# Kernel tuning notes

Measured on AMD Instinct MI355X. Metric: run time of the kernel, lower is better.

Reference implementation:

```python
import jax, jax.numpy as jnp
import numpy as np


def _reduce1(x):
    # x: [B, n, d] -> [B, 2d]; exists=max, forall=min over objects (exclude_self is a no-op for cnt=1)
    return jnp.concatenate([x.max(axis=1), x.min(axis=1)], axis=-1)


def _reduce2(x):
    # x: [B, n, n, d] -> [B, n, 2d]; exclude_self masks diagonal i==j (0 for exists/max, 1 for forall/min)
    n = x.shape[1]
    diag = jnp.eye(n, dtype=bool)[None, :, :, None]
    exists = jnp.where(diag, 0.0, x).max(axis=2)
    forall = jnp.where(diag, 1.0, x).min(axis=2)
    return jnp.concatenate([exists, forall], axis=-1)


def _layer(f0, f1, f2, p):
    # One LogicLayer step (breadth=2, minmax reducer, exclude_self, sigmoid norm, no hidden layers)
    W0, b0, W1, b1, W2, b2 = p
    B, n, d1 = f1.shape
    # order 0: [self, reduce(order1)]
    g0 = jnp.concatenate([f0, _reduce1(f1)], axis=-1)
    o0 = jax.nn.sigmoid(g0 @ W0 + b0)
    # order 1: [expand(order0), self, reduce(order2)]
    e0 = jnp.broadcast_to(f0[:, None, :], (B, n, f0.shape[-1]))
    g1 = jnp.concatenate([e0, f1, _reduce2(f2)], axis=-1)
    o1 = jax.nn.sigmoid(g1 @ W1 + b1)
    # order 2: [expand(order1), self] then Permutation(2) = cat(x, swap(i,j))
    e1 = jnp.broadcast_to(f1[:, :, None, :], (B, n, n, d1))
    g2 = jnp.concatenate([e1, f2], axis=-1)
    g2 = jnp.concatenate([g2, jnp.swapaxes(g2, 1, 2)], axis=-1)
    o2 = jax.nn.sigmoid(g2 @ W2 + b2)
    return o0, o1, o2


def setup_inputs() -> dict:
    key = jax.random.key(0)
    B, n = 4, 256
    d = [32, 64, 64]
    O = 128
    ks = iter(jax.random.split(key, 64))
    inp = {
        "x0": jax.random.uniform(next(ks), (B, d[0]), dtype=jnp.float32),
        "x1": jax.random.uniform(next(ks), (B, n, d[1]), dtype=jnp.float32),
        "x2": jax.random.uniform(next(ks), (B, n, n, d[2]), dtype=jnp.float32),
    }
    fan_ins = [
        (d[0] + 2 * d[1], d[0] + d[1] + 2 * d[2], 2 * (d[1] + d[2])),  # layer 0
        (O + 2 * O, O + O + 2 * O, 2 * (O + O)),                        # layer 1
        (O + 2 * O, O + O + 2 * O, 2 * (O + O)),                        # layer 2
    ]
    for l, fins in enumerate(fan_ins):
        for o, fin in enumerate(fins):
            inp[f"W{o}_{l}"] = jax.random.normal(next(ks), (fin, O), dtype=jnp.float32) / np.sqrt(fin).astype(np.float32)
            inp[f"b{o}_{l}"] = jnp.zeros((O,), dtype=jnp.float32)
    return inp


def reference(x0, x1, x2,
              W0_0, b0_0, W1_0, b1_0, W2_0, b2_0,
              W0_1, b0_1, W1_1, b1_1, W2_1, b2_1,
              W0_2, b0_2, W1_2, b1_2, W2_2, b2_2):
    f = (x0, x1, x2)
    for p in ((W0_0, b0_0, W1_0, b1_0, W2_0, b2_0),
              (W0_1, b0_1, W1_1, b1_1, W2_1, b2_1),
              (W0_2, b0_2, W1_2, b1_2, W2_2, b2_2)):
        f = _layer(*f, p)
    return f
```

## Files before the change

kernel.cpp:

```cpp
#include <hip/hip_runtime.h>
#include <hip/hip_bf16.h>
#include <cstdint>

#define NN 256
#define NB 4
#define OC 128

using bf16x8_t = __attribute__((ext_vector_type(8))) __bf16;
using f32x4_t  = __attribute__((ext_vector_type(4))) float;

typedef const __attribute__((address_space(1))) uint8_t* gptr1_t;
typedef __attribute__((address_space(3))) uint8_t* lptr3_t;

__device__ __forceinline__ void async_load16(const void* g, void* l) {
  __builtin_amdgcn_global_load_lds((gptr1_t)g, (lptr3_t)l, 16, 0, 0);
}

__device__ __forceinline__ float sigf(float x) {
  return 1.0f / (1.0f + __expf(-x));
}

__device__ __forceinline__ uint16_t f2bf_rne(float f) {
  uint32_t u = __float_as_uint(f);
  uint32_t r = (u + 0x7fffu + ((u >> 16) & 1u)) >> 16;
  return (uint16_t)r;
}

__global__ __launch_bounds__(256) void reduce2_l0_kernel(
    const float* __restrict__ x2, float* __restrict__ r2,
    uint16_t* __restrict__ x2bf) {
  const int bid = blockIdx.x;
  const int b = bid >> 8, i = bid & 255;
  const int tid = threadIdx.x;
  const int q = tid & 15, s = tid >> 4;
  const size_t rowbase = ((size_t)(b * NN + i) * NN) * 64 + q * 4;
  float mx0 = 0.f, mx1 = 0.f, mx2 = 0.f, mx3 = 0.f;
  float mn0 = 1.f, mn1 = 1.f, mn2 = 1.f, mn3 = 1.f;
  for (int j = s; j < NN; j += 16) {
    const float4 x = *(const float4*)(x2 + rowbase + (size_t)j * 64);
    uint2 pk;
    pk.x = (uint32_t)f2bf_rne(x.x) | ((uint32_t)f2bf_rne(x.y) << 16);
    pk.y = (uint32_t)f2bf_rne(x.z) | ((uint32_t)f2bf_rne(x.w) << 16);
    *(uint2*)(x2bf + rowbase + (size_t)j * 64) = pk;
    if (j != i) {
      mx0 = fmaxf(mx0, x.x); mx1 = fmaxf(mx1, x.y);
      mx2 = fmaxf(mx2, x.z); mx3 = fmaxf(mx3, x.w);
      mn0 = fminf(mn0, x.x); mn1 = fminf(mn1, x.y);
      mn2 = fminf(mn2, x.z); mn3 = fminf(mn3, x.w);
    }
  }
  __shared__ float4 smx[256], smn[256];
  smx[tid] = make_float4(mx0, mx1, mx2, mx3);
  smn[tid] = make_float4(mn0, mn1, mn2, mn3);
  __syncthreads();
  if (s == 0) {
    for (int ss = 1; ss < 16; ++ss) {
      float4 a = smx[q + ss * 16], c = smn[q + ss * 16];
      mx0 = fmaxf(mx0, a.x); mx1 = fmaxf(mx1, a.y);
      mx2 = fmaxf(mx2, a.z); mx3 = fmaxf(mx3, a.w);
      mn0 = fminf(mn0, c.x); mn1 = fminf(mn1, c.y);
      mn2 = fminf(mn2, c.z); mn3 = fminf(mn3, c.w);
    }
    float* r = r2 + (size_t)(b * NN + i) * 128;
    r[q * 4 + 0] = mx0; r[q * 4 + 1] = mx1; r[q * 4 + 2] = mx2; r[q * 4 + 3] = mx3;
    r[64 + q * 4 + 0] = mn0; r[64 + q * 4 + 1] = mn1;
    r[64 + q * 4 + 2] = mn2; r[64 + q * 4 + 3] = mn3;
  }
}

__global__ __launch_bounds__(256) void reduce2_bf_kernel(
    const __hip_bfloat16* __restrict__ f2, float* __restrict__ r2) {
  const int bid = blockIdx.x;
  const int b = bid >> 8, i = bid & 255;
  const int tid = threadIdx.x;
  const int q = tid & 31, s = tid >> 5;
  const size_t rowbase = ((size_t)(b * NN + i) * NN) * 128 + q * 4;
  float mx0 = 0.f, mx1 = 0.f, mx2 = 0.f, mx3 = 0.f;
  float mn0 = 1.f, mn1 = 1.f, mn2 = 1.f, mn3 = 1.f;
  for (int j = s; j < NN; j += 8) {
    const uint2 w = *(const uint2*)(f2 + rowbase + (size_t)j * 128);
    float v0 = __uint_as_float(w.x << 16);
    float v1 = __uint_as_float(w.x & 0xffff0000u);
    float v2 = __uint_as_float(w.y << 16);
    float v3 = __uint_as_float(w.y & 0xffff0000u);
    if (j != i) {
      mx0 = fmaxf(mx0, v0); mx1 = fmaxf(mx1, v1);
      mx2 = fmaxf(mx2, v2); mx3 = fmaxf(mx3, v3);
      mn0 = fminf(mn0, v0); mn1 = fminf(mn1, v1);
      mn2 = fminf(mn2, v2); mn3 = fminf(mn3, v3);
    }
  }
  __shared__ float4 smx[256], smn[256];
  smx[tid] = make_float4(mx0, mx1, mx2, mx3);
  smn[tid] = make_float4(mn0, mn1, mn2, mn3);
  __syncthreads();
  if (s == 0) {
    for (int ss = 1; ss < 8; ++ss) {
      float4 a = smx[q + ss * 32], c = smn[q + ss * 32];
      mx0 = fmaxf(mx0, a.x); mx1 = fmaxf(mx1, a.y);
      mx2 = fmaxf(mx2, a.z); mx3 = fmaxf(mx3, a.w);
      mn0 = fminf(mn0, c.x); mn1 = fminf(mn1, c.y);
      mn2 = fminf(mn2, c.z); mn3 = fminf(mn3, c.w);
    }
    float* r = r2 + (size_t)(b * NN + i) * 256;
    r[q * 4 + 0] = mx0; r[q * 4 + 1] = mx1; r[q * 4 + 2] = mx2; r[q * 4 + 3] = mx3;
    r[128 + q * 4 + 0] = mn0; r[128 + q * 4 + 1] = mn1;
    r[128 + q * 4 + 2] = mn2; r[128 + q * 4 + 3] = mn3;
  }
}

template <int D0, int D1>
__global__ __launch_bounds__(256) void o0_kernel(
    const float* __restrict__ f0, const float* __restrict__ f1,
    const float* __restrict__ W0, const float* __restrict__ b0,
    float* __restrict__ f0out) {
  constexpr int FIN = D0 + 2 * D1;
  constexpr int S = 256 / D1;
  const int b = blockIdx.x;
  const int tid = threadIdx.x;
  const int c = tid & (D1 - 1), s = tid / D1;
  __shared__ float g0[FIN];
  __shared__ float smx[256], smn[256];
  float mx = -1e30f, mn = 1e30f;
  const float* f1b = f1 + (size_t)b * NN * D1;
  for (int j = s; j < NN; j += S) {
    float x = f1b[(size_t)j * D1 + c];
    mx = fmaxf(mx, x); mn = fminf(mn, x);
  }
  smx[tid] = mx; smn[tid] = mn;
  __syncthreads();
  if (s == 0) {
    for (int ss = 1; ss < S; ++ss) {
      mx = fmaxf(mx, smx[c + ss * D1]);
      mn = fminf(mn, smn[c + ss * D1]);
    }
    g0[D0 + c] = mx;
    g0[D0 + D1 + c] = mn;
  }
  if (tid < D0) g0[tid] = f0[b * D0 + tid];
  __syncthreads();
  if (tid < OC) {
    float acc = b0[tid];
#pragma unroll 8
    for (int k = 0; k < FIN; ++k) acc += g0[k] * W0[k * OC + tid];
    f0out[b * OC + tid] = sigf(acc);
  }
}

template <int D1, int D2>
__global__ __launch_bounds__(128) void uv_kernel(
    const float* __restrict__ f1, const float* __restrict__ W2,
    const float* __restrict__ b2, float* __restrict__ u, float* __restrict__ v) {
  const int bi = blockIdx.x;
  const int c = threadIdx.x;
  const float* row = f1 + (size_t)bi * D1;
  float au = b2[c], av = 0.f;
#pragma unroll 8
  for (int k = 0; k < D1; ++k) {
    float x = row[k];
    au += x * W2[k * OC + c];
    av += x * W2[(D1 + D2 + k) * OC + c];
  }
  u[(size_t)bi * OC + c] = au;
  v[(size_t)bi * OC + c] = av;
}

template <int D0, int D1, int D2>
__global__ __launch_bounds__(128) void o1_kernel(
    const float* __restrict__ f0, const float* __restrict__ f1,
    const float* __restrict__ r2, const float* __restrict__ W1,
    const float* __restrict__ b1, float* __restrict__ f1out) {
  constexpr int FIN = D0 + D1 + 2 * D2;
  const int bi = blockIdx.x;
  const int b = bi >> 8;
  const int tid = threadIdx.x;
  __shared__ float g1[FIN];
  for (int k = tid; k < FIN; k += 128) {
    float x;
    if (k < D0) x = f0[b * D0 + k];
    else if (k < D0 + D1) x = f1[(size_t)bi * D1 + (k - D0)];
    else x = r2[(size_t)bi * (2 * D2) + (k - D0 - D1)];
    g1[k] = x;
  }
  __syncthreads();
  float acc = b1[tid];
#pragma unroll 8
  for (int k = 0; k < FIN; ++k) acc += g1[k] * W1[k * OC + tid];
  f1out[(size_t)bi * OC + tid] = sigf(acc);
}

__global__ void prep_wt_kernel(const float* __restrict__ W2,
                               uint16_t* __restrict__ Wt, int d1, int d2) {
  const int K = 2 * d2;
  const int idx = blockIdx.x * 256 + threadIdx.x;
  if (idx >= OC * K) return;
  const int nn = idx / K, k = idx - nn * K;
  const int row = (k < d2) ? (d1 + k) : (2 * d1 + d2 + (k - d2));
  Wt[idx] = f2bf_rne(W2[row * OC + nn]);
}

__device__ __forceinline__ void store_val(float* p, float x) { *p = x; }
__device__ __forceinline__ void store_val(__hip_bfloat16* p, float x) {
  *(uint16_t*)p = f2bf_rne(x);
}

template <int D2, typename OUT_T>
__global__ __launch_bounds__(256, 2) void gemm2_kernel(
    const __hip_bfloat16* __restrict__ f2, const uint16_t* __restrict__ Wt,
    const float* __restrict__ u, const float* __restrict__ v,
    OUT_T* __restrict__ out) {
  constexpr int K = 2 * D2;
  constexpr int NCH = K / 64;
  const int bid = blockIdx.x;
  const int jt = bid & 1, i = (bid >> 1) & 255, b = bid >> 9;
  const int j0 = jt * 128;
  const int tid = threadIdx.x;
  const int wv = tid >> 6, lane = tid & 63;
  const int wr = wv >> 1, wc = wv & 1;
  const int l15 = lane & 15, l4 = lane >> 4;

  __shared__ __align__(16) uint8_t ldsA[16384];
  __shared__ __align__(16) uint8_t ldsW[16384];

  const __hip_bfloat16* A1 = f2 + ((size_t)(b * NN + i) * NN + j0) * D2;
  const __hip_bfloat16* A2 = f2 + ((size_t)(b * NN + j0) * NN + i) * D2;

  f32x4_t acc[4][4];
#pragma unroll
  for (int a = 0; a < 4; ++a)
#pragma unroll
    for (int q = 0; q < 4; ++q) acc[a][q] = (f32x4_t){0.f, 0.f, 0.f, 0.f};

  for (int c = 0; c < NCH; ++c) {
    const int kbg = c * 64;
    const bool second = (kbg >= D2);
    const __hip_bfloat16* Ab = second ? A2 : A1;
    const size_t rstride = second ? (size_t)NN * D2 : (size_t)D2;
    const int kbase = second ? (kbg - D2) : kbg;
#pragma unroll
    for (int q = 0; q < 4; ++q) {
      const int id = wv * 4 + q;
      const int mi = id & 7, ks = id >> 3;
      const int row = mi * 16 + l15;
      const int kk = ks * 32 + l4 * 8;
      async_load16(Ab + (size_t)row * rstride + kbase + kk, ldsA + id * 1024);
    }
#pragma unroll
    for (int q = 0; q < 4; ++q) {
      const int id = wv * 4 + q;
      const int ni = id & 7, ks = id >> 3;
      const int nn2 = ni * 16 + l15;
      const int kk = ks * 32 + l4 * 8;
      async_load16(Wt + (size_t)nn2 * K + kbg + kk, ldsW + id * 1024);
    }
    __syncthreads();
#pragma unroll
    for (int ks = 0; ks < 2; ++ks) {
      bf16x8_t Af[4], Bf[4];
#pragma unroll
      for (int a = 0; a < 4; ++a)
        Af[a] = *(const bf16x8_t*)(ldsA + ((ks * 8 + wr * 4 + a) << 10) + (lane << 4));
#pragma unroll
      for (int q = 0; q < 4; ++q)
        Bf[q] = *(const bf16x8_t*)(ldsW + ((ks * 8 + wc * 4 + q) << 10) + (lane << 4));
#pragma unroll
      for (int a = 0; a < 4; ++a)
#pragma unroll
        for (int q = 0; q < 4; ++q)
          acc[a][q] = __builtin_amdgcn_mfma_f32_16x16x32_bf16(Af[a], Bf[q],
                                                              acc[a][q], 0, 0, 0);
    }
    __syncthreads();
  }

  const size_t uo = (size_t)(b * NN + i) * OC;
  float uval[4];
#pragma unroll
  for (int q = 0; q < 4; ++q) uval[q] = u[uo + wc * 64 + q * 16 + l15];
  const size_t obase = ((size_t)(b * NN + i) * NN + j0) * OC;
  const size_t vbase = (size_t)(b * NN + j0) * OC;
#pragma unroll
  for (int a = 0; a < 4; ++a) {
    const int rowb = wr * 64 + a * 16 + l4 * 4;
#pragma unroll
    for (int r = 0; r < 4; ++r) {
      const int j = rowb + r;
#pragma unroll
      for (int q = 0; q < 4; ++q) {
        const int col = wc * 64 + q * 16 + l15;
        const float x = acc[a][q][r] + uval[q] + v[vbase + (size_t)j * OC + col];
        store_val(out + obase + (size_t)j * OC + col, sigf(x));
      }
    }
  }
}

extern "C" void kernel_launch(void* const* d_in, const int* in_sizes, int n_in,
                              void* d_out, int out_size, void* d_ws,
                              size_t ws_size, hipStream_t stream) {
  const float* x0 = (const float*)d_in[0];
  const float* x1 = (const float*)d_in[1];
  const float* x2 = (const float*)d_in[2];
  const float *Wp[3][3], *bp[3][3];
  for (int l = 0; l < 3; ++l)
    for (int o = 0; o < 3; ++o) {
      Wp[l][o] = (const float*)d_in[3 + l * 6 + o * 2];
      bp[l][o] = (const float*)d_in[3 + l * 6 + o * 2 + 1];
    }

  const size_t F2E = (size_t)NB * NN * NN * OC;
  const size_t X2E = (size_t)NB * NN * NN * 64;

  uint8_t* ws = (uint8_t*)d_ws;
  size_t off = 0;
  auto carve = [&](size_t bytes) -> uint8_t* {
    uint8_t* p = ws + off;
    off += (bytes + 255) & ~(size_t)255;
    return p;
  };
  float* f0a = (float*)carve((size_t)NB * OC * 4);
  float* f0b = (float*)carve((size_t)NB * OC * 4);
  float* f1a = (float*)carve((size_t)NB * NN * OC * 4);
  float* f1b = (float*)carve((size_t)NB * NN * OC * 4);
  float* r2  = (float*)carve((size_t)NB * NN * 256 * 4);
  float* uu  = (float*)carve((size_t)NB * NN * OC * 4);
  float* vv  = (float*)carve((size_t)NB * NN * OC * 4);
  uint16_t* Wt0 = (uint16_t*)carve((size_t)OC * 128 * 2);
  uint16_t* Wt1 = (uint16_t*)carve((size_t)OC * 256 * 2);
  uint16_t* Wt2 = (uint16_t*)carve((size_t)OC * 256 * 2);
  __hip_bfloat16* f2a = (__hip_bfloat16*)carve(F2E * 2);

  __hip_bfloat16* f2b;
  uint16_t* x2bf;
  if (ws_size >= off + F2E * 2) {
    f2b = (__hip_bfloat16*)carve(F2E * 2);
    x2bf = (uint16_t*)f2b;
  } else {
    f2b = (__hip_bfloat16*)d_in[2];
    x2bf = (uint16_t*)carve(X2E * 2);
  }

  float* out_f0 = (float*)d_out;
  float* out_f1 = out_f0 + (size_t)NB * OC;
  float* out_f2 = out_f1 + (size_t)NB * NN * OC;

  prep_wt_kernel<<<64, 256, 0, stream>>>(Wp[0][2], Wt0, 64, 64);
  prep_wt_kernel<<<128, 256, 0, stream>>>(Wp[1][2], Wt1, 128, 128);
  prep_wt_kernel<<<128, 256, 0, stream>>>(Wp[2][2], Wt2, 128, 128);

  reduce2_l0_kernel<<<NB * NN, 256, 0, stream>>>(x2, r2, x2bf);
  o0_kernel<32, 64><<<NB, 256, 0, stream>>>(x0, x1, Wp[0][0], bp[0][0], f0a);
  uv_kernel<64, 64><<<NB * NN, 128, 0, stream>>>(x1, Wp[0][2], bp[0][2], uu, vv);
  o1_kernel<32, 64, 64><<<NB * NN, 128, 0, stream>>>(x0, x1, r2, Wp[0][1],
                                                     bp[0][1], f1a);
  gemm2_kernel<64, __hip_bfloat16><<<NB * NN * 2, 256, 0, stream>>>(
      (const __hip_bfloat16*)x2bf, Wt0, uu, vv, f2a);

  reduce2_bf_kernel<<<NB * NN, 256, 0, stream>>>(f2a, r2);
  o0_kernel<128, 128><<<NB, 256, 0, stream>>>(f0a, f1a, Wp[1][0], bp[1][0], f0b);
  uv_kernel<128, 128><<<NB * NN, 128, 0, stream>>>(f1a, Wp[1][2], bp[1][2], uu, vv);
  o1_kernel<128, 128, 128><<<NB * NN, 128, 0, stream>>>(f0a, f1a, r2, Wp[1][1],
                                                        bp[1][1], f1b);
  gemm2_kernel<128, __hip_bfloat16><<<NB * NN * 2, 256, 0, stream>>>(
      f2a, Wt1, uu, vv, f2b);

  reduce2_bf_kernel<<<NB * NN, 256, 0, stream>>>(f2b, r2);
  o0_kernel<128, 128><<<NB, 256, 0, stream>>>(f0b, f1b, Wp[2][0], bp[2][0], out_f0);
  uv_kernel<128, 128><<<NB * NN, 128, 0, stream>>>(f1b, Wp[2][2], bp[2][2], uu, vv);
  o1_kernel<128, 128, 128><<<NB * NN, 128, 0, stream>>>(f0b, f1b, r2, Wp[2][1],
                                                        bp[2][1], out_f1);
  gemm2_kernel<128, float><<<NB * NN * 2, 256, 0, stream>>>(f2b, Wt2, uu, vv,
                                                            out_f2);
}
```

Measured before the change: 632.7 us.

## Fuse order-2 reduction into GEMM epilogue and merge small per-layer kernels

The exists/forall reduction over the next layer's order-2 tensor is now computed inside the gemm2 epilogue, using LDS atomics followed by global atomic max/min on the float bit patterns. This removes two full re-reads of the bf16 f2 tensor by the separate reduce kernels. The o0, uv and o1 kernels are merged into one small_kernel that handles 4 rows per block and also initialises the next reduction buffer, and the three weight-prep launches become one. The bf16 output is staged through padded LDS for coalesced 16-byte stores, and launch bounds rise to 3 blocks per SM, which adds register pressure and atomic traffic in exchange.

```diff
diff --git a/kernel.cpp b/kernel.cpp
--- a/kernel.cpp
+++ b/kernel.cpp
@@ -68,149 +68,144 @@
   }
 }
 
-__global__ __launch_bounds__(256) void reduce2_bf_kernel(
-    const __hip_bfloat16* __restrict__ f2, float* __restrict__ r2) {
-  const int bid = blockIdx.x;
-  const int b = bid >> 8, i = bid & 255;
-  const int tid = threadIdx.x;
-  const int q = tid & 31, s = tid >> 5;
-  const size_t rowbase = ((size_t)(b * NN + i) * NN) * 128 + q * 4;
-  float mx0 = 0.f, mx1 = 0.f, mx2 = 0.f, mx3 = 0.f;
-  float mn0 = 1.f, mn1 = 1.f, mn2 = 1.f, mn3 = 1.f;
-  for (int j = s; j < NN; j += 8) {
-    const uint2 w = *(const uint2*)(f2 + rowbase + (size_t)j * 128);
-    float v0 = __uint_as_float(w.x << 16);
-    float v1 = __uint_as_float(w.x & 0xffff0000u);
-    float v2 = __uint_as_float(w.y << 16);
-    float v3 = __uint_as_float(w.y & 0xffff0000u);
-    if (j != i) {
-      mx0 = fmaxf(mx0, v0); mx1 = fmaxf(mx1, v1);
-      mx2 = fmaxf(mx2, v2); mx3 = fmaxf(mx3, v3);
-      mn0 = fminf(mn0, v0); mn1 = fminf(mn1, v1);
-      mn2 = fminf(mn2, v2); mn3 = fminf(mn3, v3);
-    }
-  }
-  __shared__ float4 smx[256], smn[256];
-  smx[tid] = make_float4(mx0, mx1, mx2, mx3);
-  smn[tid] = make_float4(mn0, mn1, mn2, mn3);
-  __syncthreads();
-  if (s == 0) {
-    for (int ss = 1; ss < 8; ++ss) {
-      float4 a = smx[q + ss * 32], c = smn[q + ss * 32];
-      mx0 = fmaxf(mx0, a.x); mx1 = fmaxf(mx1, a.y);
-      mx2 = fmaxf(mx2, a.z); mx3 = fmaxf(mx3, a.w);
-      mn0 = fminf(mn0, c.x); mn1 = fminf(mn1, c.y);
-      mn2 = fminf(mn2, c.z); mn3 = fminf(mn3, c.w);
-    }
-    float* r = r2 + (size_t)(b * NN + i) * 256;
-    r[q * 4 + 0] = mx0; r[q * 4 + 1] = mx1; r[q * 4 + 2] = mx2; r[q * 4 + 3] = mx3;
-    r[128 + q * 4 + 0] = mn0; r[128 + q * 4 + 1] = mn1;
-    r[128 + q * 4 + 2] = mn2; r[128 + q * 4 + 3] = mn3;
-  }
-}
-
-template <int D0, int D1>
-__global__ __launch_bounds__(256) void o0_kernel(
-    const float* __restrict__ f0, const float* __restrict__ f1,
-    const float* __restrict__ W0, const float* __restrict__ b0,
-    float* __restrict__ f0out) {
-  constexpr int FIN = D0 + 2 * D1;
-  constexpr int S = 256 / D1;
-  const int b = blockIdx.x;
-  const int tid = threadIdx.x;
-  const int c = tid & (D1 - 1), s = tid / D1;
-  __shared__ float g0[FIN];
-  __shared__ float smx[256], smn[256];
-  float mx = -1e30f, mn = 1e30f;
-  const float* f1b = f1 + (size_t)b * NN * D1;
-  for (int j = s; j < NN; j += S) {
-    float x = f1b[(size_t)j * D1 + c];
-    mx = fmaxf(mx, x); mn = fminf(mn, x);
-  }
-  smx[tid] = mx; smn[tid] = mn;
-  __syncthreads();
-  if (s == 0) {
-    for (int ss = 1; ss < S; ++ss) {
-      mx = fmaxf(mx, smx[c + ss * D1]);
-      mn = fminf(mn, smn[c + ss * D1]);
-    }
-    g0[D0 + c] = mx;
-    g0[D0 + D1 + c] = mn;
-  }
-  if (tid < D0) g0[tid] = f0[b * D0 + tid];
-  __syncthreads();
-  if (tid < OC) {
-    float acc = b0[tid];
-#pragma unroll 8
-    for (int k = 0; k < FIN; ++k) acc += g0[k] * W0[k * OC + tid];
-    f0out[b * OC + tid] = sigf(acc);
-  }
-}
-
-template <int D1, int D2>
-__global__ __launch_bounds__(128) void uv_kernel(
-    const float* __restrict__ f1, const float* __restrict__ W2,
-    const float* __restrict__ b2, float* __restrict__ u, float* __restrict__ v) {
-  const int bi = blockIdx.x;
-  const int c = threadIdx.x;
-  const float* row = f1 + (size_t)bi * D1;
-  float au = b2[c], av = 0.f;
-#pragma unroll 8
-  for (int k = 0; k < D1; ++k) {
-    float x = row[k];
-    au += x * W2[k * OC + c];
-    av += x * W2[(D1 + D2 + k) * OC + c];
-  }
-  u[(size_t)bi * OC + c] = au;
-  v[(size_t)bi * OC + c] = av;
-}
-
-template <int D0, int D1, int D2>
-__global__ __launch_bounds__(128) void o1_kernel(
-    const float* __restrict__ f0, const float* __restrict__ f1,
-    const float* __restrict__ r2, const float* __restrict__ W1,
-    const float* __restrict__ b1, float* __restrict__ f1out) {
-  constexpr int FIN = D0 + D1 + 2 * D2;
-  const int bi = blockIdx.x;
-  const int b = bi >> 8;
-  const int tid = threadIdx.x;
-  __shared__ float g1[FIN];
-  for (int k = tid; k < FIN; k += 128) {
-    float x;
-    if (k < D0) x = f0[b * D0 + k];
-    else if (k < D0 + D1) x = f1[(size_t)bi * D1 + (k - D0)];
-    else x = r2[(size_t)bi * (2 * D2) + (k - D0 - D1)];
-    g1[k] = x;
-  }
-  __syncthreads();
-  float acc = b1[tid];
-#pragma unroll 8
-  for (int k = 0; k < FIN; ++k) acc += g1[k] * W1[k * OC + tid];
-  f1out[(size_t)bi * OC + tid] = sigf(acc);
-}
-
-__global__ void prep_wt_kernel(const float* __restrict__ W2,
-                               uint16_t* __restrict__ Wt, int d1, int d2) {
+__device__ __forceinline__ void emit_wt(const float* __restrict__ W2,
+                                        uint16_t* __restrict__ Wt, int d1,
+                                        int d2, int idx) {
   const int K = 2 * d2;
-  const int idx = blockIdx.x * 256 + threadIdx.x;
-  if (idx >= OC * K) return;
   const int nn = idx / K, k = idx - nn * K;
   const int row = (k < d2) ? (d1 + k) : (2 * d1 + d2 + (k - d2));
   Wt[idx] = f2bf_rne(W2[row * OC + nn]);
 }
 
-__device__ __forceinline__ void store_val(float* p, float x) { *p = x; }
-__device__ __forceinline__ void store_val(__hip_bfloat16* p, float x) {
-  *(uint16_t*)p = f2bf_rne(x);
-}
-
-template <int D2, typename OUT_T>
-__global__ __launch_bounds__(256, 2) void gemm2_kernel(
+__global__ void prep_wt_all(const float* __restrict__ W20,
+                            const float* __restrict__ W21,
+                            const float* __restrict__ W22,
+                            uint16_t* __restrict__ Wt0,
+                            uint16_t* __restrict__ Wt1,
+                            uint16_t* __restrict__ Wt2) {
+  const int g = blockIdx.x * 256 + threadIdx.x;
+  if (g < 16384) emit_wt(W20, Wt0, 64, 64, g);
+  else if (g < 16384 + 32768) emit_wt(W21, Wt1, 128, 128, g - 16384);
+  else emit_wt(W22, Wt2, 128, 128, g - 49152);
+}
+
+template <int D0, int D1, int D2, bool HAS_NEXT>
+__global__ __launch_bounds__(256) void small_kernel(
+    const float* __restrict__ f0in, const float* __restrict__ f1in,
+    const float* __restrict__ r2in, const float* __restrict__ W0,
+    const float* __restrict__ b0, const float* __restrict__ W1,
+    const float* __restrict__ b1, const float* __restrict__ W2,
+    const float* __restrict__ b2, float* __restrict__ f0out,
+    float* __restrict__ f1out, float* __restrict__ u, float* __restrict__ v,
+    float* __restrict__ r2n) {
+  constexpr int FIN1 = D0 + D1 + 2 * D2;
+  constexpr int FIN0 = D0 + 2 * D1;
+  constexpr int ROWS = 4;
+  const int blk = blockIdx.x;
+  const int bi0 = blk * ROWS;
+  const int b = bi0 >> 8;
+  const int tid = threadIdx.x;
+  const int c = tid & 127, s = tid >> 7;
+
+  __shared__ float g1[ROWS][FIN1];
+  __shared__ float part[3][ROWS][2][128];
+  __shared__ float g0[FIN0];
+  __shared__ float rmx[256], rmn[256];
+
+  for (int r = 0; r < ROWS; ++r) {
+    const int bi = bi0 + r;
+    for (int k = tid; k < FIN1; k += 256) {
+      float x;
+      if (k < D0) x = f0in[b * D0 + k];
+      else if (k < D0 + D1) x = f1in[(size_t)bi * D1 + (k - D0)];
+      else x = r2in[(size_t)bi * (2 * D2) + (k - D0 - D1)];
+      g1[r][k] = x;
+    }
+  }
+  __syncthreads();
+
+  float a1[ROWS] = {0.f, 0.f, 0.f, 0.f};
+  constexpr int H1 = FIN1 / 2;
+#pragma unroll 4
+  for (int k = s * H1; k < s * H1 + H1; ++k) {
+    const float w = W1[(size_t)k * OC + c];
+#pragma unroll
+    for (int r = 0; r < ROWS; ++r) a1[r] += g1[r][k] * w;
+  }
+  float au[ROWS] = {0.f, 0.f, 0.f, 0.f};
+  float av[ROWS] = {0.f, 0.f, 0.f, 0.f};
+  constexpr int H2 = D1 / 2;
+#pragma unroll 4
+  for (int k = s * H2; k < s * H2 + H2; ++k) {
+    const float wu = W2[(size_t)k * OC + c];
+    const float wv = W2[(size_t)(D1 + D2 + k) * OC + c];
+#pragma unroll
+    for (int r = 0; r < ROWS; ++r) {
+      const float x = g1[r][D0 + k];
+      au[r] += x * wu;
+      av[r] += x * wv;
+    }
+  }
+#pragma unroll
+  for (int r = 0; r < ROWS; ++r) {
+    part[0][r][s][c] = a1[r];
+    part[1][r][s][c] = au[r];
+    part[2][r][s][c] = av[r];
+  }
+  __syncthreads();
+  if (s == 0) {
+#pragma unroll
+    for (int r = 0; r < ROWS; ++r) {
+      const size_t bi = bi0 + r;
+      f1out[bi * OC + c] = sigf(a1[r] + part[0][r][1][c] + b1[c]);
+      u[bi * OC + c] = au[r] + part[1][r][1][c] + b2[c];
+      v[bi * OC + c] = av[r] + part[2][r][1][c];
+    }
+  }
+  if (HAS_NEXT) {
+#pragma unroll
+    for (int r = 0; r < ROWS; ++r)
+      r2n[(size_t)(bi0 + r) * 256 + s * 128 + c] = (s == 0) ? 0.f : 1.f;
+  }
+
+  if ((blk & 63) == 0) {
+    constexpr int S = 256 / D1;
+    const int cc = tid & (D1 - 1), ss = tid / D1;
+    float mx = -1e30f, mn = 1e30f;
+    for (int j = ss; j < NN; j += S) {
+      const float x = f1in[((size_t)b * NN + j) * D1 + cc];
+      mx = fmaxf(mx, x); mn = fminf(mn, x);
+    }
+    rmx[tid] = mx; rmn[tid] = mn;
+    __syncthreads();
+    if (ss == 0) {
+      for (int s2 = 1; s2 < S; ++s2) {
+        mx = fmaxf(mx, rmx[cc + s2 * D1]);
+        mn = fminf(mn, rmn[cc + s2 * D1]);
+      }
+      g0[D0 + cc] = mx;
+      g0[D0 + D1 + cc] = mn;
+    }
+    if (tid < D0) g0[tid] = f0in[b * D0 + tid];
+    __syncthreads();
+    if (tid < OC) {
+      float acc = b0[tid];
+#pragma unroll 8
+      for (int k = 0; k < FIN0; ++k) acc += g0[k] * W0[k * OC + tid];
+      f0out[b * OC + tid] = sigf(acc);
+    }
+  }
+}
+
+template <int D2, typename OUT_T, bool REDUCE>
+__global__ __launch_bounds__(256, 3) void gemm2_kernel(
     const __hip_bfloat16* __restrict__ f2, const uint16_t* __restrict__ Wt,
     const float* __restrict__ u, const float* __restrict__ v,
-    OUT_T* __restrict__ out) {
+    OUT_T* __restrict__ out, float* __restrict__ r2n) {
   constexpr int K = 2 * D2;
   constexpr int NCH = K / 64;
+  constexpr bool BF16OUT = (sizeof(OUT_T) == 2);
+  constexpr int LDSB = BF16OUT ? (128 * 272) : 32768;
   const int bid = blockIdx.x;
   const int jt = bid & 1, i = (bid >> 1) & 255, b = bid >> 9;
   const int j0 = jt * 128;
@@ -219,8 +214,10 @@
   const int wr = wv >> 1, wc = wv & 1;
   const int l15 = lane & 15, l4 = lane >> 4;
 
-  __shared__ __align__(16) uint8_t ldsA[16384];
-  __shared__ __align__(16) uint8_t ldsW[16384];
+  __shared__ __align__(16) uint8_t lds[LDSB];
+  __shared__ unsigned smax[128], smin[128];
+  uint8_t* const ldsA = lds;
+  uint8_t* const ldsW = lds + 16384;
 
   const __hip_bfloat16* A1 = f2 + ((size_t)(b * NN + i) * NN + j0) * D2;
   const __hip_bfloat16* A2 = f2 + ((size_t)(b * NN + j0) * NN + i) * D2;
@@ -273,23 +270,74 @@
     __syncthreads();
   }
 
-  const size_t uo = (size_t)(b * NN + i) * OC;
+  const size_t bi2 = (size_t)(b * NN + i);
   float uval[4];
 #pragma unroll
-  for (int q = 0; q < 4; ++q) uval[q] = u[uo + wc * 64 + q * 16 + l15];
-  const size_t obase = ((size_t)(b * NN + i) * NN + j0) * OC;
+  for (int q = 0; q < 4; ++q) uval[q] = u[bi2 * OC + wc * 64 + q * 16 + l15];
+  const size_t obase = (bi2 * NN + j0) * OC;
   const size_t vbase = (size_t)(b * NN + j0) * OC;
-#pragma unroll
-  for (int a = 0; a < 4; ++a) {
-    const int rowb = wr * 64 + a * 16 + l4 * 4;
-#pragma unroll
-    for (int r = 0; r < 4; ++r) {
-      const int j = rowb + r;
+
+  if (BF16OUT) {
+    if (REDUCE && tid < 128) { smax[tid] = 0u; smin[tid] = 0x3f800000u; }
+    __syncthreads();
+    float lmx[4] = {0.f, 0.f, 0.f, 0.f};
+    float lmn[4] = {1.f, 1.f, 1.f, 1.f};
+#pragma unroll
+    for (int a = 0; a < 4; ++a) {
+      const int rowb = wr * 64 + a * 16 + l4 * 4;
+#pragma unroll
+      for (int r = 0; r < 4; ++r) {
+        const int j = rowb + r;
+        const bool excl = (j0 + j) == i;
+#pragma unroll
+        for (int q = 0; q < 4; ++q) {
+          const int col = wc * 64 + q * 16 + l15;
+          const float x = acc[a][q][r] + uval[q] + v[vbase + (size_t)j * OC + col];
+          const float sg = sigf(x);
+          *(uint16_t*)(lds + j * 272 + col * 2) = f2bf_rne(sg);
+          if (REDUCE && !excl) {
+            lmx[q] = fmaxf(lmx[q], sg);
+            lmn[q] = fminf(lmn[q], sg);
+          }
+        }
+      }
+    }
+    if (REDUCE) {
 #pragma unroll
       for (int q = 0; q < 4; ++q) {
         const int col = wc * 64 + q * 16 + l15;
-        const float x = acc[a][q][r] + uval[q] + v[vbase + (size_t)j * OC + col];
-        store_val(out + obase + (size_t)j * OC + col, sigf(x));
+        atomicMax(&smax[col], __float_as_uint(lmx[q]));
+        atomicMin(&smin[col], __float_as_uint(lmn[q]));
+      }
+    }
+    __syncthreads();
+    uint16_t* const outp = (uint16_t*)out;
+#pragma unroll
+    for (int ci = 0; ci < 8; ++ci) {
+      const int chunk = ci * 256 + tid;
+      const int row = chunk >> 4, off = chunk & 15;
+      const uint4 val = *(const uint4*)(lds + row * 272 + off * 16);
+      *(uint4*)(outp + obase + (size_t)row * OC + off * 8) = val;
+    }
+    if (REDUCE && tid < 128) {
+      unsigned* const r2u = (unsigned*)r2n;
+      atomicMax(&r2u[bi2 * 256 + tid], smax[tid]);
+      atomicMin(&r2u[bi2 * 256 + 128 + tid], smin[tid]);
+    }
+  } else {
+    float* const outp = (float*)out;
+#pragma unroll
+    for (int a = 0; a < 4; ++a) {
+      const int rowb = wr * 64 + a * 16 + l4 * 4;
+#pragma unroll
+      for (int r = 0; r < 4; ++r) {
+        const int j = rowb + r;
+#pragma unroll
+        for (int q = 0; q < 4; ++q) {
+          const int col = wc * 64 + q * 16 + l15;
+          const float x = acc[a][q][r] + uval[q] + v[vbase + (size_t)j * OC + col];
+          outp[obase + (size_t)j * OC + col] = sigf(x);
+        }
       }
     }
   }
@@ -322,7 +370,9 @@
   float* f0b = (float*)carve((size_t)NB * OC * 4);
   float* f1a = (float*)carve((size_t)NB * NN * OC * 4);
   float* f1b = (float*)carve((size_t)NB * NN * OC * 4);
-  float* r2  = (float*)carve((size_t)NB * NN * 256 * 4);
+  float* r2a = (float*)carve((size_t)NB * NN * 128 * 4);
+  float* r2b = (float*)carve((size_t)NB * NN * 256 * 4);
+  float* r2c = (float*)carve((size_t)NB * NN * 256 * 4);
   float* uu  = (float*)carve((size_t)NB * NN * OC * 4);
   float* vv  = (float*)carve((size_t)NB * NN * OC * 4);
   uint16_t* Wt0 = (uint16_t*)carve((size_t)OC * 128 * 2);
@@ -344,31 +394,25 @@
   float* out_f1 = out_f0 + (size_t)NB * OC;
   float* out_f2 = out_f1 + (size_t)NB * NN * OC;
 
-  prep_wt_kernel<<<64, 256, 0, stream>>>(Wp[0][2], Wt0, 64, 64);
-  prep_wt_kernel<<<128, 256, 0, stream>>>(Wp[1][2], Wt1, 128, 128);
-  prep_wt_kernel<<<128, 256, 0, stream>>>(Wp[2][2], Wt2, 128, 128);
-
-  reduce2_l0_kernel<<<NB * NN, 256, 0, stream>>>(x2, r2, x2bf);
-  o0_kernel<32, 64><<<NB, 256, 0, stream>>>(x0, x1, Wp[0][0], bp[0][0], f0a);
-  uv_kernel<64, 64><<<NB * NN, 128, 0, stream>>>(x1, Wp[0][2], bp[0][2], uu, vv);
-  o1_kernel<32, 64, 64><<<NB * NN, 128, 0, stream>>>(x0, x1, r2, Wp[0][1],
-                                                     bp[0][1], f1a);
-  gemm2_kernel<64, __hip_bfloat16><<<NB * NN * 2, 256, 0, stream>>>(
-      (const __hip_bfloat16*)x2bf, Wt0, uu, vv, f2a);
-
-  reduce2_bf_kernel<<<NB * NN, 256, 0, stream>>>(f2a, r2);
-  o0_kernel<128, 128><<<NB, 256, 0, stream>>>(f0a, f1a, Wp[1][0], bp[1][0], f0b);
-  uv_kernel<128, 128><<<NB * NN, 128, 0, stream>>>(f1a, Wp[1][2], bp[1][2], uu, vv);
-  o1_kernel<128, 128, 128><<<NB * NN, 128, 0, stream>>>(f0a, f1a, r2, Wp[1][1],
-                                                        bp[1][1], f1b);
-  gemm2_kernel<128, __hip_bfloat16><<<NB * NN * 2, 256, 0, stream>>>(
-      f2a, Wt1, uu, vv, f2b);
-
-  reduce2_bf_kernel<<<NB * NN, 256, 0, stream>>>(f2b, r2);
-  o0_kernel<128, 128><<<NB, 256, 0, stream>>>(f0b, f1b, Wp[2][0], bp[2][0], out_f0);
-  uv_kernel<128, 128><<<NB * NN, 128, 0, stream>>>(f1b, Wp[2][2], bp[2][2], uu, vv);
-  o1_kernel<128, 128, 128><<<NB * NN, 128, 0, stream>>>(f0b, f1b, r2, Wp[2][1],
-                                                        bp[2][1], out_f1);
-  gemm2_kernel<128, float><<<NB * NN * 2, 256, 0, stream>>>(f2b, Wt2, uu, vv,
-                                                            out_f2);
-}
+  prep_wt_all<<<320, 256, 0, stream>>>(Wp[0][2], Wp[1][2], Wp[2][2], Wt0, Wt1,
+                                       Wt2);
+  reduce2_l0_kernel<<<NB * NN, 256, 0, stream>>>(x2, r2a, x2bf);
+
+  small_kernel<32, 64, 64, true><<<NB * NN / 4, 256, 0, stream>>>(
+      x0, x1, r2a, Wp[0][0], bp[0][0], Wp[0][1], bp[0][1], Wp[0][2], bp[0][2],
+      f0a, f1a, uu, vv, r2b);
+  gemm2_kernel<64, __hip_bfloat16, true><<<NB * NN * 2, 256, 0, stream>>>(
+      (const __hip_bfloat16*)x2bf, Wt0, uu, vv, f2a, r2b);
+
+  small_kernel<128, 128, 128, true><<<NB * NN / 4, 256, 0, stream>>>(
+      f0a, f1a, r2b, Wp[1][0], bp[1][0], Wp[1][1], bp[1][1], Wp[1][2], bp[1][2],
+      f0b, f1b, uu, vv, r2c);
+  gemm2_kernel<128, __hip_bfloat16, true><<<NB * NN * 2, 256, 0, stream>>>(
+      f2a, Wt1, uu, vv, f2b, r2c);
+
+  small_kernel<128, 128, 128, false><<<NB * NN / 4, 256, 0, stream>>>(
+      f0b, f1b, r2c, Wp[2][0], bp[2][0], Wp[2][1], bp[2][1], Wp[2][2], bp[2][2],
+      out_f0, out_f1, uu, vv, nullptr);
+  gemm2_kernel<128, float, false><<<NB * NN * 2, 256, 0, stream>>>(
+      f2b, Wt2, uu, vv, out_f2, nullptr);
+}
```

Result: faster. 584.8 us (-7.6%).
